# Optimization experiments

Hardware: AMD Instinct MI355X
Metric: run time of the kernel (lower is better)

The kernel has to match this reference:

```python
import jax, jax.numpy as jnp
import numpy as np

N = 50000      # nodes
E = 800000     # edges (avg degree 16)
D = 128        # in_dim = hidden_dim
C = 40         # num_classes
BN_EPS = 1e-5


def setup_inputs() -> dict:
    key = jax.random.key(0)
    ks = jax.random.split(key, 24)
    h = jax.random.normal(ks[0], (N, D), dtype=jnp.float32)
    edge_src = jax.random.randint(ks[1], (E,), 0, N)
    edge_dst = jax.random.randint(ks[2], (E,), 0, N)
    mask = jnp.ones((E, 1), dtype=jnp.float32)  # adj_mask2_fixed (frozen)

    def lin_w(k, fi, fo):
        return jax.random.normal(k, (fi, fo), dtype=jnp.float32) / np.sqrt(fi).astype(np.float32)

    def lin_b(k, fo):
        return jax.random.normal(k, (fo,), dtype=jnp.float32) * 0.01

    dims = [(D, D), (D, D), (D, C)]  # last GIN layer -> num_classes
    out = {"h": h, "edge_src": edge_src, "edge_dst": edge_dst, "mask": mask}
    for i, (fi, fo) in enumerate(dims):
        out[f"w{i}"] = lin_w(ks[3 + 4 * i], fi, fo)
        out[f"b{i}"] = lin_b(ks[4 + 4 * i], fo)
        out[f"g{i}"] = jnp.ones((fo,), jnp.float32) + 0.05 * jax.random.normal(ks[5 + 4 * i], (fo,), jnp.float32)
        out[f"beta{i}"] = 0.05 * jax.random.normal(ks[6 + 4 * i], (fo,), jnp.float32)
        out[f"rm{i}"] = 0.1 * jax.random.normal(jax.random.fold_in(key, 100 + i), (fo,), jnp.float32)
        out[f"rv{i}"] = jax.random.uniform(jax.random.fold_in(key, 200 + i), (fo,), jnp.float32, 0.5, 1.5)
    out["wp"] = lin_w(ks[20], D, C)
    out["bp"] = lin_b(ks[21], C)
    return out


def reference(h, edge_src, edge_dst, mask,
              w0, b0, g0, beta0, rm0, rv0,
              w1, b1, g1, beta1, rm1, rv1,
              w2, b2, g2, beta2, rm2, rv2,
              wp, bp):
    # in-degree for mean aggregation (DGL mean reducer: divide by in-degree,
    # zero for isolated nodes)
    ones_e = jnp.ones(edge_dst.shape, dtype=h.dtype)
    deg = jax.ops.segment_sum(ones_e, edge_dst, num_segments=N)
    deg_inv = jnp.where(deg > 0, 1.0 / jnp.maximum(deg, 1.0), 0.0)[:, None]

    def gin_layer(x, w, b, g, beta, rm, rv):
        msg = x[edge_src] * mask                                   # [E, d]
        agg = jax.ops.segment_sum(msg, edge_dst, num_segments=N) * deg_inv
        z = (x + agg) @ w + b                                      # (1+eps)=1, eps=0
        z = (z - rm) * jax.lax.rsqrt(rv + BN_EPS) * g + beta       # BN (eval, running stats)
        return jax.nn.relu(z)                                      # dropout: eval -> identity

    h1 = gin_layer(h, w0, b0, g0, beta0, rm0, rv0)    # [N, D]
    h2 = gin_layer(h1, w1, b1, g1, beta1, rm1, rv1)   # [N, D]  hidden_rep[-2]
    h3 = gin_layer(h2, w2, b2, g2, beta2, rm2, rv2)   # [N, C]  hidden_rep[-1]
    return ((h2 @ wp + bp) + h3) * 0.5
```

## Files before the change

### kernel.cpp

```cpp
#include <hip/hip_runtime.h>

#define N_NODES 50000
#define N_EDGES 800000
#define DIM 128
#define NCLS 40

#define NCHUNK 128
#define CE 6250
#define HALF_N 25088
#define WHALF 12544
#define SCAN_B 98
#define N_PAD 50432

typedef __bf16 bf16x8_t __attribute__((ext_vector_type(8)));
typedef unsigned short us8_t __attribute__((ext_vector_type(8)));
typedef float f32x4_t __attribute__((ext_vector_type(4)));

static __device__ __forceinline__ float b2f(unsigned short h) {
    unsigned u = ((unsigned)h) << 16;
    return __builtin_bit_cast(float, u);
}
static __device__ __forceinline__ unsigned short f2b(float f) {
    unsigned u = __builtin_bit_cast(unsigned, f);
    u += 0x7FFFu + ((u >> 16) & 1u);
    return (unsigned short)(u >> 16);
}

__global__ __launch_bounds__(256) void to_bf16(const float* __restrict__ in,
                                               unsigned short* __restrict__ out) {
    size_t e0 = ((size_t)blockIdx.x * 256 + threadIdx.x) * 8;
    f32x4_t v0 = *(const f32x4_t*)(in + e0);
    f32x4_t v1 = *(const f32x4_t*)(in + e0 + 4);
    us8_t o;
    #pragma unroll
    for (int j = 0; j < 4; ++j) { o[j] = f2b(v0[j]); o[4 + j] = f2b(v1[j]); }
    *(us8_t*)(out + e0) = o;
}

__global__ __launch_bounds__(256) void repack_w(const float* __restrict__ w0,
                                                const float* __restrict__ w1,
                                                const float* __restrict__ w2,
                                                const float* __restrict__ wp,
                                                unsigned short* __restrict__ f0h,
                                                unsigned short* __restrict__ f0l,
                                                unsigned short* __restrict__ f1h,
                                                unsigned short* __restrict__ f1l,
                                                unsigned short* __restrict__ f2h,
                                                unsigned short* __restrict__ f2l,
                                                unsigned short* __restrict__ fph,
                                                unsigned short* __restrict__ fpl) {
    int t = blockIdx.x * 256 + threadIdx.x;
    const float* src;
    unsigned short *dh, *dl;
    int idx, ncols;
    if (t < 16384)      { src = w0; dh = f0h; dl = f0l; idx = t;         ncols = 128; }
    else if (t < 32768) { src = w1; dh = f1h; dl = f1l; idx = t - 16384; ncols = 128; }
    else if (t < 38912) { src = w2; dh = f2h; dl = f2l; idx = t - 32768; ncols = 48; }
    else if (t < 45056) { src = wp; dh = fph; dl = fpl; idx = t - 38912; ncols = 48; }
    else return;
    int k = idx / ncols, n = idx - k * ncols;
    float v;
    if (ncols == 128) v = src[k * 128 + n];
    else              v = (n < NCLS) ? src[k * NCLS + n] : 0.f;
    int nt = n >> 4, m = n & 15, kt = k >> 5, quad = (k >> 3) & 3, j = k & 7;
    int off = ((nt * 4 + kt) * 64 + quad * 16 + m) * 8 + j;
    unsigned short hi = f2b(v);
    dh[off] = hi;
    dl[off] = f2b(v - b2f(hi));
}

__global__ __launch_bounds__(256) void chunk_count(const int* __restrict__ dst,
                                                   unsigned* __restrict__ cnt) {
    __shared__ unsigned lds[WHALF];
    int c = blockIdx.x, h = blockIdx.y, tid = threadIdx.x;
    for (int w = tid; w < WHALF; w += 256) lds[w] = 0;
    __syncthreads();
    int base = c * CE;
    for (int k = tid; k < CE; k += 256) {
        int local = dst[base + k] - h * HALF_N;
        if (local >= 0 && local < HALF_N)
            atomicAdd(&lds[local >> 1], 1u << ((local & 1) * 16));
    }
    __syncthreads();
    unsigned* out = cnt + ((size_t)(h * NCHUNK + c)) * WHALF;
    for (int w = tid; w < WHALF; w += 256) out[w] = lds[w];
}

__global__ __launch_bounds__(256) void cscan(unsigned* __restrict__ cnt,
                                             unsigned* __restrict__ degp,
                                             int* __restrict__ partial) {
    __shared__ int lds[256];
    int b = blockIdx.x;
    int h = b / 49;
    int w = (b % 49) * 256 + threadIdx.x;
    unsigned acc = 0;
    for (int c = 0; c < NCHUNK; ++c) {
        size_t idx = ((size_t)(h * NCHUNK + c)) * WHALF + w;
        unsigned v = cnt[idx];
        cnt[idx] = acc;
        acc += v;
    }
    degp[h * WHALF + w] = acc;
    lds[threadIdx.x] = (int)(acc & 0xFFFFu) + (int)(acc >> 16);
    __syncthreads();
    #pragma unroll
    for (int off = 128; off > 0; off >>= 1) {
        if (threadIdx.x < off) lds[threadIdx.x] += lds[threadIdx.x + off];
        __syncthreads();
    }
    if (threadIdx.x == 0) partial[b] = lds[0];
}

__global__ __launch_bounds__(128) void scan_blocks(const int* __restrict__ partial,
                                                   int* __restrict__ blk_off) {
    __shared__ int lds[128];
    int tid = threadIdx.x;
    lds[tid] = (tid < SCAN_B) ? partial[tid] : 0;
    __syncthreads();
    #pragma unroll
    for (int off = 1; off < 128; off <<= 1) {
        int v = lds[tid];
        int add = (tid >= off) ? lds[tid - off] : 0;
        __syncthreads();
        lds[tid] = v + add;
        __syncthreads();
    }
    if (tid < SCAN_B) blk_off[tid] = (tid == 0) ? 0 : lds[tid - 1];
}

__global__ __launch_bounds__(256) void scan_final(const unsigned* __restrict__ degp,
                                                  const int* __restrict__ blk_off,
                                                  int* __restrict__ rs,
                                                  int* __restrict__ deg,
                                                  float* __restrict__ dinv) {
    __shared__ int lds[256];
    int b = blockIdx.x;
    int h = b / 49;
    int tid = threadIdx.x;
    int w = (b % 49) * 256 + tid;
    unsigned dp = degp[h * WHALF + w];
    int lo = (int)(dp & 0xFFFFu), hi = (int)(dp >> 16);
    int s = lo + hi;
    lds[tid] = s;
    __syncthreads();
    #pragma unroll
    for (int off = 1; off < 256; off <<= 1) {
        int v = lds[tid];
        int add = (tid >= off) ? lds[tid - off] : 0;
        __syncthreads();
        lds[tid] = v + add;
        __syncthreads();
    }
    int excl = blk_off[b] + lds[tid] - s;
    int n0 = h * HALF_N + 2 * w;
    rs[n0] = excl;
    rs[n0 + 1] = excl + lo;
    deg[n0] = lo;
    deg[n0 + 1] = hi;
    dinv[n0] = (lo > 0) ? (1.0f / (float)lo) : 0.0f;
    dinv[n0 + 1] = (hi > 0) ? (1.0f / (float)hi) : 0.0f;
}

__global__ __launch_bounds__(256) void fill2(const int* __restrict__ src,
                                             const int* __restrict__ dst,
                                             const float* __restrict__ mask,
                                             const unsigned* __restrict__ cnt,
                                             const int* __restrict__ rs,
                                             unsigned* __restrict__ csr) {
    __shared__ unsigned cur[WHALF];
    int c = blockIdx.x, h = blockIdx.y, tid = threadIdx.x;
    const unsigned* off = cnt + ((size_t)(h * NCHUNK + c)) * WHALF;
    for (int w = tid; w < WHALF; w += 256) cur[w] = off[w];
    __syncthreads();
    int base = c * CE;
    for (int k = tid; k < CE; k += 256) {
        int e = base + k;
        int d = dst[e];
        int local = d - h * HALF_N;
        if (local >= 0 && local < HALF_N) {
            unsigned sm = (unsigned)src[e] | ((unsigned)f2b(mask[e]) << 16);
            int sh = (local & 1) * 16;
            unsigned old = atomicAdd(&cur[local >> 1], 1u << sh);
            int rank = (int)((old >> sh) & 0xFFFFu);
            csr[rs[d] + rank] = sm;
        }
    }
}

__global__ __launch_bounds__(256) void agg_kernel(const unsigned short* __restrict__ xb,
                                                  const float* __restrict__ x,
                                                  float* __restrict__ xin,
                                                  const int* __restrict__ rs,
                                                  const int* __restrict__ deg,
                                                  const float* __restrict__ dinv,
                                                  const unsigned* __restrict__ csr) {
    int lane = threadIdx.x & 63;
    int node = blockIdx.x * 4 + (threadIdx.x >> 6);
    if (node >= N_NODES) return;
    int cnt = deg[node];
    int start = rs[node];
    float acc0 = 0.f, acc1 = 0.f;
    for (int base = 0; base < cnt; base += 16) {
        int nb = cnt - base;
        if (nb > 16) nb = 16;
        unsigned pk = 0;
        if (lane < nb) pk = csr[start + base + lane];
        unsigned vv[16];
        float mm[16];
        #pragma unroll
        for (int j = 0; j < 16; ++j) {
            unsigned p = (unsigned)__builtin_amdgcn_readlane((int)pk, j);
            mm[j] = b2f((unsigned short)(p >> 16));
            vv[j] = *(const unsigned*)(xb + (size_t)(p & 0xFFFFu) * DIM + lane * 2);
        }
        #pragma unroll
        for (int j = 0; j < 16; ++j) {
            acc0 += mm[j] * b2f((unsigned short)(vv[j] & 0xFFFFu));
            acc1 += mm[j] * b2f((unsigned short)(vv[j] >> 16));
        }
    }
    float di = dinv[node];
    float2 xp = *(const float2*)(x + (size_t)node * DIM + lane * 2);
    float2 o;
    o.x = xp.x + acc0 * di;
    o.y = xp.y + acc1 * di;
    *(float2*)(xin + (size_t)node * DIM + lane * 2) = o;
}

__global__ __launch_bounds__(256) void gemm128_bn_relu(const float* __restrict__ xin,
                                                       const unsigned short* __restrict__ wfh,
                                                       const unsigned short* __restrict__ wfl,
                                                       const float* __restrict__ bias,
                                                       const float* __restrict__ gam,
                                                       const float* __restrict__ bet,
                                                       const float* __restrict__ rm,
                                                       const float* __restrict__ rv,
                                                       float* __restrict__ out,
                                                       unsigned short* __restrict__ outb) {
    int tid = threadIdx.x;
    int wave = tid >> 6, lane = tid & 63;
    int m = lane & 15, quad = lane >> 4;
    int rbase = blockIdx.x * 64 + wave * 16;
    int arow = rbase + m;
    const float* ap = xin + (size_t)(arow < N_NODES ? arow : 0) * DIM;

    us8_t ah[4], al[4];
    #pragma unroll
    for (int kt = 0; kt < 4; ++kt) {
        f32x4_t p0 = *(const f32x4_t*)(ap + kt * 32 + quad * 8);
        f32x4_t p1 = *(const f32x4_t*)(ap + kt * 32 + quad * 8 + 4);
        #pragma unroll
        for (int j = 0; j < 4; ++j) {
            unsigned short h0 = f2b(p0[j]);
            unsigned short h1 = f2b(p1[j]);
            ah[kt][j] = h0;
            ah[kt][4 + j] = h1;
            al[kt][j] = f2b(p0[j] - b2f(h0));
            al[kt][4 + j] = f2b(p1[j] - b2f(h1));
        }
    }

    f32x4_t acc[8] = {};
    #pragma unroll
    for (int kt = 0; kt < 4; ++kt) {
        #pragma unroll
        for (int nt = 0; nt < 8; ++nt) {
            int boff = ((nt * 4 + kt) * 64 + lane) * 8;
            us8_t bh = *(const us8_t*)(wfh + boff);
            us8_t bl = *(const us8_t*)(wfl + boff);
            acc[nt] = __builtin_amdgcn_mfma_f32_16x16x32_bf16(
                __builtin_bit_cast(bf16x8_t, ah[kt]),
                __builtin_bit_cast(bf16x8_t, bh), acc[nt], 0, 0, 0);
            acc[nt] = __builtin_amdgcn_mfma_f32_16x16x32_bf16(
                __builtin_bit_cast(bf16x8_t, ah[kt]),
                __builtin_bit_cast(bf16x8_t, bl), acc[nt], 0, 0, 0);
            acc[nt] = __builtin_amdgcn_mfma_f32_16x16x32_bf16(
                __builtin_bit_cast(bf16x8_t, al[kt]),
                __builtin_bit_cast(bf16x8_t, bh), acc[nt], 0, 0, 0);
        }
    }

    #pragma unroll
    for (int nt = 0; nt < 8; ++nt) {
        int j = nt * 16 + m;
        float bj = bias[j];
        float sc = gam[j] * rsqrtf(rv[j] + 1e-5f);
        float sh = bet[j] - rm[j] * sc;
        #pragma unroll
        for (int i = 0; i < 4; ++i) {
            int r = rbase + quad * 4 + i;
            if (r < N_NODES) {
                float z = fmaxf((acc[nt][i] + bj) * sc + sh, 0.f);
                out[(size_t)r * DIM + j] = z;
                outb[(size_t)r * DIM + j] = f2b(z);
            }
        }
    }
}

__global__ __launch_bounds__(256) void fused_final(const float* __restrict__ xin2,
                                                   const float* __restrict__ h2,
                                                   const unsigned short* __restrict__ f2h,
                                                   const unsigned short* __restrict__ f2l,
                                                   const unsigned short* __restrict__ fph,
                                                   const unsigned short* __restrict__ fpl,
                                                   const float* __restrict__ b2,
                                                   const float* __restrict__ g2,
                                                   const float* __restrict__ be2,
                                                   const float* __restrict__ rm2,
                                                   const float* __restrict__ rv2,
                                                   const float* __restrict__ bp,
                                                   float* __restrict__ out) {
    int tid = threadIdx.x;
    int wave = tid >> 6, lane = tid & 63;
    int m = lane & 15, quad = lane >> 4;
    int rbase = blockIdx.x * 64 + wave * 16;
    int arow = rbase + m;
    size_t rowoff = (size_t)(arow < N_NODES ? arow : 0) * DIM;
    const float* ap2 = xin2 + rowoff;
    const float* aph = h2 + rowoff;

    us8_t a2h[4], a2l[4], ahh[4], ahl[4];
    #pragma unroll
    for (int kt = 0; kt < 4; ++kt) {
        f32x4_t p0 = *(const f32x4_t*)(ap2 + kt * 32 + quad * 8);
        f32x4_t p1 = *(const f32x4_t*)(ap2 + kt * 32 + quad * 8 + 4);
        f32x4_t q0 = *(const f32x4_t*)(aph + kt * 32 + quad * 8);
        f32x4_t q1 = *(const f32x4_t*)(aph + kt * 32 + quad * 8 + 4);
        #pragma unroll
        for (int j = 0; j < 4; ++j) {
            unsigned short h0 = f2b(p0[j]), h1 = f2b(p1[j]);
            a2h[kt][j] = h0; a2h[kt][4 + j] = h1;
            a2l[kt][j] = f2b(p0[j] - b2f(h0));
            a2l[kt][4 + j] = f2b(p1[j] - b2f(h1));
            unsigned short g0 = f2b(q0[j]), g1 = f2b(q1[j]);
            ahh[kt][j] = g0; ahh[kt][4 + j] = g1;
            ahl[kt][j] = f2b(q0[j] - b2f(g0));
            ahl[kt][4 + j] = f2b(q1[j] - b2f(g1));
        }
    }

    f32x4_t acc2[3] = {};
    f32x4_t accp[3] = {};
    #pragma unroll
    for (int kt = 0; kt < 4; ++kt) {
        #pragma unroll
        for (int nt = 0; nt < 3; ++nt) {
            int boff = ((nt * 4 + kt) * 64 + lane) * 8;
            us8_t b2hv = *(const us8_t*)(f2h + boff);
            us8_t b2lv = *(const us8_t*)(f2l + boff);
            us8_t bphv = *(const us8_t*)(fph + boff);
            us8_t bplv = *(const us8_t*)(fpl + boff);
            acc2[nt] = __builtin_amdgcn_mfma_f32_16x16x32_bf16(
                __builtin_bit_cast(bf16x8_t, a2h[kt]),
                __builtin_bit_cast(bf16x8_t, b2hv), acc2[nt], 0, 0, 0);
            acc2[nt] = __builtin_amdgcn_mfma_f32_16x16x32_bf16(
                __builtin_bit_cast(bf16x8_t, a2h[kt]),
                __builtin_bit_cast(bf16x8_t, b2lv), acc2[nt], 0, 0, 0);
            acc2[nt] = __builtin_amdgcn_mfma_f32_16x16x32_bf16(
                __builtin_bit_cast(bf16x8_t, a2l[kt]),
                __builtin_bit_cast(bf16x8_t, b2hv), acc2[nt], 0, 0, 0);
            accp[nt] = __builtin_amdgcn_mfma_f32_16x16x32_bf16(
                __builtin_bit_cast(bf16x8_t, ahh[kt]),
                __builtin_bit_cast(bf16x8_t, bphv), accp[nt], 0, 0, 0);
            accp[nt] = __builtin_amdgcn_mfma_f32_16x16x32_bf16(
                __builtin_bit_cast(bf16x8_t, ahh[kt]),
                __builtin_bit_cast(bf16x8_t, bplv), accp[nt], 0, 0, 0);
            accp[nt] = __builtin_amdgcn_mfma_f32_16x16x32_bf16(
                __builtin_bit_cast(bf16x8_t, ahl[kt]),
                __builtin_bit_cast(bf16x8_t, bphv), accp[nt], 0, 0, 0);
        }
    }

    #pragma unroll
    for (int nt = 0; nt < 3; ++nt) {
        int j = nt * 16 + m;
        int jc = (j < NCLS) ? j : (NCLS - 1);
        float b2j = b2[jc];
        float sc = g2[jc] * rsqrtf(rv2[jc] + 1e-5f);
        float sh = be2[jc] - rm2[jc] * sc;
        float bpj = bp[jc];
        #pragma unroll
        for (int i = 0; i < 4; ++i) {
            int r = rbase + quad * 4 + i;
            if (r < N_NODES && j < NCLS) {
                float z = fmaxf((acc2[nt][i] + b2j) * sc + sh, 0.f);
                float p = accp[nt][i] + bpj;
                out[(size_t)r * NCLS + j] = (p + z) * 0.5f;
            }
        }
    }
}

extern "C" void kernel_launch(void* const* d_in, const int* in_sizes, int n_in,
                              void* d_out, int out_size, void* d_ws, size_t ws_size,
                              hipStream_t stream) {
    const float* h    = (const float*)d_in[0];
    const int* esrc   = (const int*)d_in[1];
    const int* edst   = (const int*)d_in[2];
    const float* mask = (const float*)d_in[3];
    const float* w0   = (const float*)d_in[4];
    const float* b0   = (const float*)d_in[5];
    const float* g0   = (const float*)d_in[6];
    const float* be0  = (const float*)d_in[7];
    const float* rm0  = (const float*)d_in[8];
    const float* rv0  = (const float*)d_in[9];
    const float* w1   = (const float*)d_in[10];
    const float* b1   = (const float*)d_in[11];
    const float* g1   = (const float*)d_in[12];
    const float* be1  = (const float*)d_in[13];
    const float* rm1  = (const float*)d_in[14];
    const float* rv1  = (const float*)d_in[15];
    const float* w2   = (const float*)d_in[16];
    const float* b2   = (const float*)d_in[17];
    const float* g2   = (const float*)d_in[18];
    const float* be2  = (const float*)d_in[19];
    const float* rm2  = (const float*)d_in[20];
    const float* rv2  = (const float*)d_in[21];
    const float* wp   = (const float*)d_in[22];
    const float* bp   = (const float*)d_in[23];

    char* ws = (char*)d_ws;
    size_t off = 0;
    auto alloc = [&](size_t bytes) {
        char* p = ws + off;
        off = (off + bytes + 255) & ~(size_t)255;
        return p;
    };
    int* rs       = (int*)alloc(N_PAD * 4);
    int* deg      = (int*)alloc(N_PAD * 4);
    float* dinv   = (float*)alloc(N_PAD * 4);
    int* partial  = (int*)alloc(128 * 4);
    int* blk_off  = (int*)alloc(128 * 4);
    unsigned* degp = (unsigned*)alloc(2 * WHALF * 4);
    unsigned* csr = (unsigned*)alloc((size_t)N_EDGES * 4);
    float* xin    = (float*)alloc((size_t)N_NODES * DIM * 4);
    float* hb     = (float*)alloc((size_t)N_NODES * DIM * 4);
    unsigned short* xb16 = (unsigned short*)alloc((size_t)N_NODES * DIM * 2);
    unsigned short* hb16 = (unsigned short*)alloc((size_t)N_NODES * DIM * 2);
    unsigned short* f0h = (unsigned short*)alloc(16384 * 2);
    unsigned short* f0l = (unsigned short*)alloc(16384 * 2);
    unsigned short* f1h = (unsigned short*)alloc(16384 * 2);
    unsigned short* f1l = (unsigned short*)alloc(16384 * 2);
    unsigned short* f2h = (unsigned short*)alloc(6144 * 2);
    unsigned short* f2l = (unsigned short*)alloc(6144 * 2);
    unsigned short* fph = (unsigned short*)alloc(6144 * 2);
    unsigned short* fpl = (unsigned short*)alloc(6144 * 2);
    unsigned* cnt = (unsigned*)xin;

    const int AB = (N_NODES + 3) / 4;
    const int GB = (N_NODES + 63) / 64;

    to_bf16<<<3125, 256, 0, stream>>>(h, xb16);
    repack_w<<<176, 256, 0, stream>>>(w0, w1, w2, wp, f0h, f0l, f1h, f1l,
                                      f2h, f2l, fph, fpl);
    chunk_count<<<dim3(NCHUNK, 2), 256, 0, stream>>>(edst, cnt);
    cscan<<<SCAN_B, 256, 0, stream>>>(cnt, degp, partial);
    scan_blocks<<<1, 128, 0, stream>>>(partial, blk_off);
    scan_final<<<SCAN_B, 256, 0, stream>>>(degp, blk_off, rs, deg, dinv);
    fill2<<<dim3(NCHUNK, 2), 256, 0, stream>>>(esrc, edst, mask, cnt, rs, csr);

    agg_kernel<<<AB, 256, 0, stream>>>(xb16, h, xin, rs, deg, dinv, csr);
    gemm128_bn_relu<<<GB, 256, 0, stream>>>(xin, f0h, f0l, b0, g0, be0, rm0, rv0, hb, hb16);
    agg_kernel<<<AB, 256, 0, stream>>>(hb16, hb, xin, rs, deg, dinv, csr);
    gemm128_bn_relu<<<GB, 256, 0, stream>>>(xin, f1h, f1l, b1, g1, be1, rm1, rv1, hb, hb16);
    agg_kernel<<<AB, 256, 0, stream>>>(hb16, hb, xin, rs, deg, dinv, csr);
    fused_final<<<GB, 256, 0, stream>>>(xin, hb, f2h, f2l, fph, fpl,
                                        b2, g2, be2, rm2, rv2, bp, (float*)d_out);
}
```

Baseline: 328.6 us.

## Fuse neighbor aggregation into GEMM kernels via shared-memory row staging

Merges the aggregation kernel into the per-layer GEMM+BN+ReLU kernel and the final kernel. Each 64-row block first gathers its 16 rows per wave into LDS, then runs the MFMA GEMM from LDS. This removes the fp32 xin round trip through global memory and three launches. The gather now uses 32-edge batches with guarded sub-chunks. The cost is lower parallelism, since one wave handles 16 nodes sequentially with 768 blocks instead of 12500. About 33KB of LDS per block also limits occupancy. Separate ping-pong activation buffers and a dedicated cnt buffer are added because xin is gone.

Measured after the change: 450.4 us. 37.1% more time.

```diff
diff --git a/kernel.cpp b/kernel.cpp
--- a/kernel.cpp
+++ b/kernel.cpp
@@ -11,6 +11,8 @@
 #define WHALF 12544
 #define SCAN_B 98
 #define N_PAD 50432
+
+#define ROWP 132
 
 typedef __bf16 bf16x8_t __attribute__((ext_vector_type(8)));
 typedef unsigned short us8_t __attribute__((ext_vector_type(8)));
@@ -187,68 +189,89 @@
     }
 }
 
-__global__ __launch_bounds__(256) void agg_kernel(const unsigned short* __restrict__ xb,
-                                                  const float* __restrict__ x,
-                                                  float* __restrict__ xin,
-                                                  const int* __restrict__ rs,
-                                                  const int* __restrict__ deg,
-                                                  const float* __restrict__ dinv,
-                                                  const unsigned* __restrict__ csr) {
-    int lane = threadIdx.x & 63;
-    int node = blockIdx.x * 4 + (threadIdx.x >> 6);
-    if (node >= N_NODES) return;
-    int cnt = deg[node];
-    int start = rs[node];
-    float acc0 = 0.f, acc1 = 0.f;
-    for (int base = 0; base < cnt; base += 16) {
-        int nb = cnt - base;
-        if (nb > 16) nb = 16;
-        unsigned pk = 0;
-        if (lane < nb) pk = csr[start + base + lane];
-        unsigned vv[16];
-        float mm[16];
-        #pragma unroll
-        for (int j = 0; j < 16; ++j) {
-            unsigned p = (unsigned)__builtin_amdgcn_readlane((int)pk, j);
-            mm[j] = b2f((unsigned short)(p >> 16));
-            vv[j] = *(const unsigned*)(xb + (size_t)(p & 0xFFFFu) * DIM + lane * 2);
-        }
-        #pragma unroll
-        for (int j = 0; j < 16; ++j) {
-            acc0 += mm[j] * b2f((unsigned short)(vv[j] & 0xFFFFu));
-            acc1 += mm[j] * b2f((unsigned short)(vv[j] >> 16));
-        }
-    }
-    float di = dinv[node];
-    float2 xp = *(const float2*)(x + (size_t)node * DIM + lane * 2);
-    float2 o;
-    o.x = xp.x + acc0 * di;
-    o.y = xp.y + acc1 * di;
-    *(float2*)(xin + (size_t)node * DIM + lane * 2) = o;
-}
-
-__global__ __launch_bounds__(256) void gemm128_bn_relu(const float* __restrict__ xin,
-                                                       const unsigned short* __restrict__ wfh,
-                                                       const unsigned short* __restrict__ wfl,
-                                                       const float* __restrict__ bias,
-                                                       const float* __restrict__ gam,
-                                                       const float* __restrict__ bet,
-                                                       const float* __restrict__ rm,
-                                                       const float* __restrict__ rv,
-                                                       float* __restrict__ out,
-                                                       unsigned short* __restrict__ outb) {
+static __device__ __forceinline__ void gather_rows(float* arow,
+                                                   const unsigned short* __restrict__ xb,
+                                                   const float* __restrict__ xres,
+                                                   const int* __restrict__ rs,
+                                                   const int* __restrict__ deg,
+                                                   const float* __restrict__ dinv,
+                                                   const unsigned* __restrict__ csr,
+                                                   int rbase, int wave, int lane) {
+    for (int i = 0; i < 16; ++i) {
+        int node = rbase + wave * 16 + i;
+        if (node >= N_NODES) continue;
+        int cntn = deg[node];
+        int start = rs[node];
+        float acc0 = 0.f, acc1 = 0.f;
+        for (int base = 0; base < cntn; base += 32) {
+            int nb = cntn - base;
+            if (nb > 32) nb = 32;
+            unsigned pk = 0;
+            if (lane < nb) pk = csr[start + base + lane];
+            unsigned vv[32];
+            float mm[32];
+            #pragma unroll
+            for (int j8 = 0; j8 < 4; ++j8) {
+                if (j8 * 8 < nb) {
+                    #pragma unroll
+                    for (int j = j8 * 8; j < j8 * 8 + 8; ++j) {
+                        unsigned p = (unsigned)__builtin_amdgcn_readlane((int)pk, j);
+                        mm[j] = b2f((unsigned short)(p >> 16));
+                        vv[j] = *(const unsigned*)(xb + (size_t)(p & 0xFFFFu) * DIM + lane * 2);
+                    }
+                }
+            }
+            #pragma unroll
+            for (int j8 = 0; j8 < 4; ++j8) {
+                if (j8 * 8 < nb) {
+                    #pragma unroll
+                    for (int j = j8 * 8; j < j8 * 8 + 8; ++j) {
+                        acc0 += mm[j] * b2f((unsigned short)(vv[j] & 0xFFFFu));
+                        acc1 += mm[j] * b2f((unsigned short)(vv[j] >> 16));
+                    }
+                }
+            }
+        }
+        float di = dinv[node];
+        float2 xp = *(const float2*)(xres + (size_t)node * DIM + lane * 2);
+        float2 o;
+        o.x = xp.x + acc0 * di;
+        o.y = xp.y + acc1 * di;
+        *(float2*)&arow[(wave * 16 + i) * ROWP + lane * 2] = o;
+    }
+}
+
+__global__ __launch_bounds__(256) void fused_gin(const unsigned short* __restrict__ xb,
+                                                 const float* __restrict__ xres,
+                                                 const int* __restrict__ rs,
+                                                 const int* __restrict__ deg,
+                                                 const float* __restrict__ dinv,
+                                                 const unsigned* __restrict__ csr,
+                                                 const unsigned short* __restrict__ wfh,
+                                                 const unsigned short* __restrict__ wfl,
+                                                 const float* __restrict__ bias,
+                                                 const float* __restrict__ gam,
+                                                 const float* __restrict__ bet,
+                                                 const float* __restrict__ rm,
+                                                 const float* __restrict__ rv,
+                                                 float* __restrict__ out,
+                                                 unsigned short* __restrict__ outb) {
+    __shared__ float arow[64 * ROWP];
     int tid = threadIdx.x;
     int wave = tid >> 6, lane = tid & 63;
+    int rbase = blockIdx.x * 64;
+
+    gather_rows(arow, xb, xres, rs, deg, dinv, csr, rbase, wave, lane);
+    __syncthreads();
+
     int m = lane & 15, quad = lane >> 4;
-    int rbase = blockIdx.x * 64 + wave * 16;
-    int arow = rbase + m;
-    const float* ap = xin + (size_t)(arow < N_NODES ? arow : 0) * DIM;
+    const float* arp = &arow[(wave * 16 + m) * ROWP];
 
     us8_t ah[4], al[4];
     #pragma unroll
     for (int kt = 0; kt < 4; ++kt) {
-        f32x4_t p0 = *(const f32x4_t*)(ap + kt * 32 + quad * 8);
-        f32x4_t p1 = *(const f32x4_t*)(ap + kt * 32 + quad * 8 + 4);
+        f32x4_t p0 = *(const f32x4_t*)(arp + kt * 32 + quad * 8);
+        f32x4_t p1 = *(const f32x4_t*)(arp + kt * 32 + quad * 8 + 4);
         #pragma unroll
         for (int j = 0; j < 4; ++j) {
             unsigned short h0 = f2b(p0[j]);
@@ -280,6 +303,7 @@
         }
     }
 
+    int rb = rbase + wave * 16;
     #pragma unroll
     for (int nt = 0; nt < 8; ++nt) {
         int j = nt * 16 + m;
@@ -288,7 +312,7 @@
         float sh = bet[j] - rm[j] * sc;
         #pragma unroll
         for (int i = 0; i < 4; ++i) {
-            int r = rbase + quad * 4 + i;
+            int r = rb + quad * 4 + i;
             if (r < N_NODES) {
                 float z = fmaxf((acc[nt][i] + bj) * sc + sh, 0.f);
                 out[(size_t)r * DIM + j] = z;
@@ -298,8 +322,12 @@
     }
 }
 
-__global__ __launch_bounds__(256) void fused_final(const float* __restrict__ xin2,
+__global__ __launch_bounds__(256) void fused_final(const unsigned short* __restrict__ xb,
                                                    const float* __restrict__ h2,
+                                                   const int* __restrict__ rs,
+                                                   const int* __restrict__ deg,
+                                                   const float* __restrict__ dinv,
+                                                   const unsigned* __restrict__ csr,
                                                    const unsigned short* __restrict__ f2h,
                                                    const unsigned short* __restrict__ f2l,
                                                    const unsigned short* __restrict__ fph,
@@ -311,20 +339,24 @@
                                                    const float* __restrict__ rv2,
                                                    const float* __restrict__ bp,
                                                    float* __restrict__ out) {
+    __shared__ float arow[64 * ROWP];
     int tid = threadIdx.x;
     int wave = tid >> 6, lane = tid & 63;
+    int rbase = blockIdx.x * 64;
+
+    gather_rows(arow, xb, h2, rs, deg, dinv, csr, rbase, wave, lane);
+    __syncthreads();
+
     int m = lane & 15, quad = lane >> 4;
-    int rbase = blockIdx.x * 64 + wave * 16;
-    int arow = rbase + m;
-    size_t rowoff = (size_t)(arow < N_NODES ? arow : 0) * DIM;
-    const float* ap2 = xin2 + rowoff;
-    const float* aph = h2 + rowoff;
+    const float* arp = &arow[(wave * 16 + m) * ROWP];
+    int arow_g = rbase + wave * 16 + m;
+    const float* aph = h2 + (size_t)(arow_g < N_NODES ? arow_g : 0) * DIM;
 
     us8_t a2h[4], a2l[4], ahh[4], ahl[4];
     #pragma unroll
     for (int kt = 0; kt < 4; ++kt) {
-        f32x4_t p0 = *(const f32x4_t*)(ap2 + kt * 32 + quad * 8);
-        f32x4_t p1 = *(const f32x4_t*)(ap2 + kt * 32 + quad * 8 + 4);
+        f32x4_t p0 = *(const f32x4_t*)(arp + kt * 32 + quad * 8);
+        f32x4_t p1 = *(const f32x4_t*)(arp + kt * 32 + quad * 8 + 4);
         f32x4_t q0 = *(const f32x4_t*)(aph + kt * 32 + quad * 8);
         f32x4_t q1 = *(const f32x4_t*)(aph + kt * 32 + quad * 8 + 4);
         #pragma unroll
@@ -372,6 +404,7 @@
         }
     }
 
+    int rb = rbase + wave * 16;
     #pragma unroll
     for (int nt = 0; nt < 3; ++nt) {
         int j = nt * 16 + m;
@@ -382,7 +415,7 @@
         float bpj = bp[jc];
         #pragma unroll
         for (int i = 0; i < 4; ++i) {
-            int r = rbase + quad * 4 + i;
+            int r = rb + quad * 4 + i;
             if (r < N_NODES && j < NCLS) {
                 float z = fmaxf((acc2[nt][i] + b2j) * sc + sh, 0.f);
                 float p = accp[nt][i] + bpj;
@@ -433,11 +466,13 @@
     int* partial  = (int*)alloc(128 * 4);
     int* blk_off  = (int*)alloc(128 * 4);
     unsigned* degp = (unsigned*)alloc(2 * WHALF * 4);
+    unsigned* cnt = (unsigned*)alloc((size_t)2 * NCHUNK * WHALF * 4);
     unsigned* csr = (unsigned*)alloc((size_t)N_EDGES * 4);
-    float* xin    = (float*)alloc((size_t)N_NODES * DIM * 4);
-    float* hb     = (float*)alloc((size_t)N_NODES * DIM * 4);
-    unsigned short* xb16 = (unsigned short*)alloc((size_t)N_NODES * DIM * 2);
-    unsigned short* hb16 = (unsigned short*)alloc((size_t)N_NODES * DIM * 2);
+    float* hbA    = (float*)alloc((size_t)N_NODES * DIM * 4);
+    float* hbB    = (float*)alloc((size_t)N_NODES * DIM * 4);
+    unsigned short* xb16  = (unsigned short*)alloc((size_t)N_NODES * DIM * 2);
+    unsigned short* hbA16 = (unsigned short*)alloc((size_t)N_NODES * DIM * 2);
+    unsigned short* hbB16 = (unsigned short*)alloc((size_t)N_NODES * DIM * 2);
     unsigned short* f0h = (unsigned short*)alloc(16384 * 2);
     unsigned short* f0l = (unsigned short*)alloc(16384 * 2);
     unsigned short* f1h = (unsigned short*)alloc(16384 * 2);
@@ -446,9 +481,7 @@
     unsigned short* f2l = (unsigned short*)alloc(6144 * 2);
     unsigned short* fph = (unsigned short*)alloc(6144 * 2);
     unsigned short* fpl = (unsigned short*)alloc(6144 * 2);
-    unsigned* cnt = (unsigned*)xin;
-
-    const int AB = (N_NODES + 3) / 4;
+
     const int GB = (N_NODES + 63) / 64;
 
     to_bf16<<<3125, 256, 0, stream>>>(h, xb16);
@@ -460,11 +493,11 @@
     scan_final<<<SCAN_B, 256, 0, stream>>>(degp, blk_off, rs, deg, dinv);
     fill2<<<dim3(NCHUNK, 2), 256, 0, stream>>>(esrc, edst, mask, cnt, rs, csr);
 
-    agg_kernel<<<AB, 256, 0, stream>>>(xb16, h, xin, rs, deg, dinv, csr);
-    gemm128_bn_relu<<<GB, 256, 0, stream>>>(xin, f0h, f0l, b0, g0, be0, rm0, rv0, hb, hb16);
-    agg_kernel<<<AB, 256, 0, stream>>>(hb16, hb, xin, rs, deg, dinv, csr);
-    gemm128_bn_relu<<<GB, 256, 0, stream>>>(xin, f1h, f1l, b1, g1, be1, rm1, rv1, hb, hb16);
-    agg_kernel<<<AB, 256, 0, stream>>>(hb16, hb, xin, rs, deg, dinv, csr);
-    fused_final<<<GB, 256, 0, stream>>>(xin, hb, f2h, f2l, fph, fpl,
+    fused_gin<<<GB, 256, 0, stream>>>(xb16, h, rs, deg, dinv, csr,
+                                      f0h, f0l, b0, g0, be0, rm0, rv0, hbA, hbA16);
+    fused_gin<<<GB, 256, 0, stream>>>(hbA16, hbA, rs, deg, dinv, csr,
+                                      f1h, f1l, b1, g1, be1, rm1, rv1, hbB, hbB16);
+    fused_final<<<GB, 256, 0, stream>>>(hbB16, hbB, rs, deg, dinv, csr,
+                                        f2h, f2l, fph, fpl,
                                         b2, g2, be2, rm2, rv2, bp, (float*)d_out);
 }
```

## Record per-edge ranks during counting and fill CSR with a flat edge-parallel kernel

Applied to the files above, without the earlier changes.

The counting pass now stores each edge's intra-chunk rank from the LDS atomic, so the fill pass no longer redoes LDS atomics or reloads per-chunk offset tables into shared memory. The fill becomes one thread per edge that reads the chunk offset word, the row start and the stored rank to compute the CSR slot. The chunk count is halved, so the count and scan passes handle fewer per-chunk tables. In exchange it adds a 1.6MB rank buffer write and read, and fill3 does scattered global reads of the offset table.

New measurement: 334.3 us. No clear change (+1.8%).

```diff
diff --git a/kernel.cpp b/kernel.cpp
--- a/kernel.cpp
+++ b/kernel.cpp
@@ -5,8 +5,8 @@
 #define DIM 128
 #define NCLS 40
 
-#define NCHUNK 128
-#define CE 6250
+#define NCHUNK 64
+#define CE 12500
 #define HALF_N 25088
 #define WHALF 12544
 #define SCAN_B 98
@@ -70,16 +70,21 @@
 }
 
 __global__ __launch_bounds__(256) void chunk_count(const int* __restrict__ dst,
-                                                   unsigned* __restrict__ cnt) {
+                                                   unsigned* __restrict__ cnt,
+                                                   unsigned short* __restrict__ ranks) {
     __shared__ unsigned lds[WHALF];
     int c = blockIdx.x, h = blockIdx.y, tid = threadIdx.x;
     for (int w = tid; w < WHALF; w += 256) lds[w] = 0;
     __syncthreads();
     int base = c * CE;
     for (int k = tid; k < CE; k += 256) {
-        int local = dst[base + k] - h * HALF_N;
-        if (local >= 0 && local < HALF_N)
-            atomicAdd(&lds[local >> 1], 1u << ((local & 1) * 16));
+        int e = base + k;
+        int local = dst[e] - h * HALF_N;
+        if (local >= 0 && local < HALF_N) {
+            int sh = (local & 1) * 16;
+            unsigned old = atomicAdd(&lds[local >> 1], 1u << sh);
+            ranks[e] = (unsigned short)((old >> sh) & 0xFFFFu);
+        }
     }
     __syncthreads();
     unsigned* out = cnt + ((size_t)(h * NCHUNK + c)) * WHALF;
@@ -161,30 +166,23 @@
     dinv[n0 + 1] = (hi > 0) ? (1.0f / (float)hi) : 0.0f;
 }
 
-__global__ __launch_bounds__(256) void fill2(const int* __restrict__ src,
+__global__ __launch_bounds__(256) void fill3(const int* __restrict__ src,
                                              const int* __restrict__ dst,
                                              const float* __restrict__ mask,
                                              const unsigned* __restrict__ cnt,
                                              const int* __restrict__ rs,
+                                             const unsigned short* __restrict__ ranks,
                                              unsigned* __restrict__ csr) {
-    __shared__ unsigned cur[WHALF];
-    int c = blockIdx.x, h = blockIdx.y, tid = threadIdx.x;
-    const unsigned* off = cnt + ((size_t)(h * NCHUNK + c)) * WHALF;
-    for (int w = tid; w < WHALF; w += 256) cur[w] = off[w];
-    __syncthreads();
-    int base = c * CE;
-    for (int k = tid; k < CE; k += 256) {
-        int e = base + k;
-        int d = dst[e];
-        int local = d - h * HALF_N;
-        if (local >= 0 && local < HALF_N) {
-            unsigned sm = (unsigned)src[e] | ((unsigned)f2b(mask[e]) << 16);
-            int sh = (local & 1) * 16;
-            unsigned old = atomicAdd(&cur[local >> 1], 1u << sh);
-            int rank = (int)((old >> sh) & 0xFFFFu);
-            csr[rs[d] + rank] = sm;
-        }
-    }
+    int e = blockIdx.x * 256 + threadIdx.x;
+    if (e >= N_EDGES) return;
+    int d = dst[e];
+    int c = e / CE;
+    int h = (d >= HALF_N) ? 1 : 0;
+    int local = d - h * HALF_N;
+    int sh = (local & 1) * 16;
+    unsigned cw = cnt[((size_t)(h * NCHUNK + c)) * WHALF + (local >> 1)];
+    int pos = rs[d] + (int)((cw >> sh) & 0xFFFFu) + (int)ranks[e];
+    csr[pos] = (unsigned)src[e] | ((unsigned)f2b(mask[e]) << 16);
 }
 
 __global__ __launch_bounds__(256) void agg_kernel(const unsigned short* __restrict__ xb,
@@ -434,6 +432,7 @@
     int* blk_off  = (int*)alloc(128 * 4);
     unsigned* degp = (unsigned*)alloc(2 * WHALF * 4);
     unsigned* csr = (unsigned*)alloc((size_t)N_EDGES * 4);
+    unsigned short* ranks = (unsigned short*)alloc((size_t)N_EDGES * 2);
     float* xin    = (float*)alloc((size_t)N_NODES * DIM * 4);
     float* hb     = (float*)alloc((size_t)N_NODES * DIM * 4);
     unsigned short* xb16 = (unsigned short*)alloc((size_t)N_NODES * DIM * 2);
@@ -448,17 +447,18 @@
     unsigned short* fpl = (unsigned short*)alloc(6144 * 2);
     unsigned* cnt = (unsigned*)xin;
 
+    const int EB = (N_EDGES + 255) / 256;
     const int AB = (N_NODES + 3) / 4;
     const int GB = (N_NODES + 63) / 64;
 
     to_bf16<<<3125, 256, 0, stream>>>(h, xb16);
     repack_w<<<176, 256, 0, stream>>>(w0, w1, w2, wp, f0h, f0l, f1h, f1l,
                                       f2h, f2l, fph, fpl);
-    chunk_count<<<dim3(NCHUNK, 2), 256, 0, stream>>>(edst, cnt);
+    chunk_count<<<dim3(NCHUNK, 2), 256, 0, stream>>>(edst, cnt, ranks);
     cscan<<<SCAN_B, 256, 0, stream>>>(cnt, degp, partial);
     scan_blocks<<<1, 128, 0, stream>>>(partial, blk_off);
     scan_final<<<SCAN_B, 256, 0, stream>>>(degp, blk_off, rs, deg, dinv);
-    fill2<<<dim3(NCHUNK, 2), 256, 0, stream>>>(esrc, edst, mask, cnt, rs, csr);
+    fill3<<<EB, 256, 0, stream>>>(esrc, edst, mask, cnt, rs, ranks, csr);
 
     agg_kernel<<<AB, 256, 0, stream>>>(xb16, h, xin, rs, deg, dinv, csr);
     gemm128_bn_relu<<<GB, 256, 0, stream>>>(xin, f0h, f0l, b0, g0, be0, rm0, rv0, hb, hb16);
```
